# Performance work log

Measured on AMD Instinct MI355X. Metric: run time of the kernel, lower is better.

Reference implementation:

```python
import jax, jax.numpy as jnp
import numpy as np

B, C, M = 64, 64, 8192
EPS = 1e-05

def setup_inputs() -> dict:
    key = jax.random.key(0)
    x = jax.random.normal(key, (B, C, M), dtype=jnp.float32)
    return {"x": x}

def _mT(a):
    return jnp.swapaxes(a, -1, -2)

def reference(x):
    b, c, m = x.shape
    mu = x.mean(axis=2, keepdims=True)
    xc = x - mu
    cov = (xc @ _mT(xc)) / m                      # (B,C,C)
    # RBLW shrinkage
    I = jnp.eye(c, dtype=x.dtype)[None]
    trace = jnp.trace(cov, axis1=-2, axis2=-1)[:, None, None]
    second_trace = jnp.einsum('bij,bji->b', cov, cov)[:, None, None]
    numerator = (m - 2) / m * second_trace + trace ** 2
    denominator = (m + 2) * (second_trace - trace ** 2 / c)
    rho = jnp.minimum(numerator / denominator, 1.0)
    F_hat = trace / c * I
    cov = rho * F_hat + (1 - rho) * cov + EPS * I
    # eigen decomposition (no-grad in original)
    covs = jax.lax.stop_gradient(cov)
    U, L, _ = jnp.linalg.svd(covs)                # U:(B,C,C) L:(B,C) descending
    ratio = jnp.cumsum(L, axis=1) / jnp.sum(L, axis=1, keepdims=True)
    conds = jnp.any(ratio >= 1 - EPS, axis=0) | jnp.any(L <= EPS, axis=0)  # (C,)
    counter = jnp.where(jnp.any(conds), jnp.argmax(conds), c)
    # iterative rank-1 eigen refinement + deflation via scan with break mask
    Ucols = jnp.moveaxis(U, 2, 0)[..., None]      # (C,B,C,1)
    Lcols = L.T                                    # (C,B)
    S0 = jnp.zeros_like(cov)

    def step(carry, inp):
        cov_c, S_hat, active = carry
        v, Lj, j = inp                            # v:(B,C,1), Lj:(B,)
        step_active = active & (j < counter)
        # power_layer forward is identity on v
        vt = _mT(v)
        lam = (vt @ cov_c @ v) / (vt @ v)         # (B,1,1)
        Lj = Lj[:, None, None]
        ok = step_active & (~jnp.any(lam < 0)) & (~jnp.any(jnp.abs(lam - Lj) / Lj > 0.1))
        lam_safe = jnp.where(ok, lam, jnp.ones_like(lam))
        vvT = v @ vt
        S_hat = S_hat + jnp.where(ok, jax.lax.rsqrt(lam_safe) * vvT, 0.0)
        cov_c = jnp.where(ok, cov_c - cov_c @ vvT, cov_c)
        return (cov_c, S_hat, ok), None

    (_, S_hat, _), _ = jax.lax.scan(step, (cov, S0, jnp.array(True)),
                                    (Ucols, Lcols, jnp.arange(c)))
    Z = S_hat @ xc
    return Z
```

## Files before the change

kernel.cpp:

```cpp
#include <hip/hip_runtime.h>
#include <math.h>

#define BB 64
#define CCH 64
#define MMH 8192
#define SLICES 8
#define KSL 1024
#define KCH 128
#define TMZ 64
constexpr double EPSV = 1e-5;

typedef __attribute__((ext_vector_type(8))) short bf16x8;
typedef __attribute__((ext_vector_type(8))) unsigned short u16x8;
typedef __attribute__((ext_vector_type(16))) float floatx16;

__global__ __launch_bounds__(256, 2) void k1_partG(const float* __restrict__ x,
                                                   float* __restrict__ Gpart,
                                                   float* __restrict__ rspart) {
  __shared__ unsigned short h1[64][KCH + 8], h2[64][KCH + 8], h3[64][KCH + 8];
  __shared__ float rred[64][4];
  const int tid = threadIdx.x;
  const int b = blockIdx.x / SLICES;
  const int s = blockIdx.x % SLICES;
  const int row = tid >> 2;
  const int seg = (tid & 3) * 32;
  const int wv = tid >> 6;
  const int lane = tid & 63;
  const int rw = wv >> 1, cw = wv & 1;
  const int mrow = 32 * rw + (lane & 31);
  const int ncol = 32 * cw + (lane & 31);
  const int koff = (lane >> 5) * 8;
  const float* xb = x + (size_t)b * CCH * MMH + (size_t)s * KSL;
  floatx16 acc = {};
  float rsum = 0.f;
  for (int c = 0; c < KSL / KCH; ++c) {
    const float* xp = xb + (size_t)row * MMH + c * KCH + seg;
    float v[32];
#pragma unroll
    for (int q = 0; q < 8; ++q) {
      float4 t = *(const float4*)(xp + 4 * q);
      v[4 * q] = t.x;
      v[4 * q + 1] = t.y;
      v[4 * q + 2] = t.z;
      v[4 * q + 3] = t.w;
    }
#pragma unroll
    for (int o = 0; o < 32; ++o) rsum += v[o];
#pragma unroll
    for (int g = 0; g < 4; ++g) {
      u16x8 a1, a2, a3;
#pragma unroll
      for (int j = 0; j < 8; ++j) {
        float f = v[8 * g + j];
        unsigned u = __float_as_uint(f);
        unsigned short q1 = (unsigned short)(u >> 16);
        float r1 = f - __uint_as_float(u & 0xffff0000u);
        unsigned u1 = __float_as_uint(r1);
        unsigned short q2 = (unsigned short)(u1 >> 16);
        float r2 = r1 - __uint_as_float(u1 & 0xffff0000u);
        unsigned short q3 = (unsigned short)(__float_as_uint(r2) >> 16);
        a1[j] = q1;
        a2[j] = q2;
        a3[j] = q3;
      }
      *(u16x8*)&h1[row][seg + 8 * g] = a1;
      *(u16x8*)&h2[row][seg + 8 * g] = a2;
      *(u16x8*)&h3[row][seg + 8 * g] = a3;
    }
    __syncthreads();
#pragma unroll
    for (int ks = 0; ks < KCH / 16; ++ks) {
      const int kk = ks * 16 + koff;
      bf16x8 A1 = *(const bf16x8*)&h1[mrow][kk];
      bf16x8 A2 = *(const bf16x8*)&h2[mrow][kk];
      bf16x8 A3 = *(const bf16x8*)&h3[mrow][kk];
      bf16x8 B1 = *(const bf16x8*)&h1[ncol][kk];
      bf16x8 B2 = *(const bf16x8*)&h2[ncol][kk];
      bf16x8 B3 = *(const bf16x8*)&h3[ncol][kk];
      acc = __builtin_amdgcn_mfma_f32_32x32x16_bf16(A1, B1, acc, 0, 0, 0);
      acc = __builtin_amdgcn_mfma_f32_32x32x16_bf16(A1, B2, acc, 0, 0, 0);
      acc = __builtin_amdgcn_mfma_f32_32x32x16_bf16(A2, B1, acc, 0, 0, 0);
      acc = __builtin_amdgcn_mfma_f32_32x32x16_bf16(A2, B2, acc, 0, 0, 0);
      acc = __builtin_amdgcn_mfma_f32_32x32x16_bf16(A1, B3, acc, 0, 0, 0);
      acc = __builtin_amdgcn_mfma_f32_32x32x16_bf16(A3, B1, acc, 0, 0, 0);
    }
    __syncthreads();
  }
  float* gp = Gpart + ((size_t)(b * SLICES + s)) * 4096;
#pragma unroll
  for (int r = 0; r < 16; ++r) {
    int row32 = (r & 3) + 8 * (r >> 2) + 4 * (lane >> 5);
    gp[(32 * rw + row32) * 64 + 32 * cw + (lane & 31)] = acc[r];
  }
  rred[row][tid & 3] = rsum;
  __syncthreads();
  if (tid < 64) {
    rspart[((size_t)(b * SLICES + s)) * 64 + tid] =
        rred[tid][0] + rred[tid][1] + rred[tid][2] + rred[tid][3];
  }
}

__global__ __launch_bounds__(256) void k2_reduce(const float* __restrict__ Gpart,
                                                 const float* __restrict__ rspart,
                                                 float* __restrict__ cov32,
                                                 float* __restrict__ mu32,
                                                 double* __restrict__ scal) {
  __shared__ double muS[64];
  __shared__ double red[256];
  const int tid = threadIdx.x;
  const int b = blockIdx.x;
  if (tid < 64) {
    double r = 0.0;
    for (int s = 0; s < SLICES; ++s) r += (double)rspart[((size_t)(b * SLICES + s)) * 64 + tid];
    double mu = r / (double)MMH;
    muS[tid] = mu;
    mu32[b * 64 + tid] = (float)mu;
  }
  __syncthreads();
  const int base = tid * 16;
  const int i = tid >> 2;
  double g[16];
#pragma unroll
  for (int e = 0; e < 16; ++e) g[e] = 0.0;
  for (int s = 0; s < SLICES; ++s) {
    const float* gp = Gpart + ((size_t)(b * SLICES + s)) * 4096 + base;
#pragma unroll
    for (int q = 0; q < 4; ++q) {
      float4 t = *(const float4*)(gp + 4 * q);
      g[4 * q] += (double)t.x;
      g[4 * q + 1] += (double)t.y;
      g[4 * q + 2] += (double)t.z;
      g[4 * q + 3] += (double)t.w;
    }
  }
  double t1 = 0.0, t2 = 0.0;
#pragma unroll
  for (int e = 0; e < 16; ++e) {
    int j = (base + e) & 63;
    double cv = g[e] / (double)MMH - muS[i] * muS[j];
    cov32[(size_t)b * 4096 + base + e] = (float)cv;
    if (i == j) t1 += cv;
    t2 += cv * cv;
  }
  red[tid] = t1;
  __syncthreads();
  for (int st = 128; st > 0; st >>= 1) {
    if (tid < st) red[tid] += red[tid + st];
    __syncthreads();
  }
  double T1 = red[0];
  __syncthreads();
  red[tid] = t2;
  __syncthreads();
  for (int st = 128; st > 0; st >>= 1) {
    if (tid < st) red[tid] += red[tid + st];
    __syncthreads();
  }
  double T2 = red[0];
  if (tid == 0) {
    double num = ((double)(MMH - 2) / (double)MMH) * T2 + T1 * T1;
    double den = (double)(MMH + 2) * (T2 - T1 * T1 / (double)CCH);
    double r = num / den;
    double rho = (r < 1.0) ? r : 1.0;
    scal[b * 4 + 0] = rho;
    scal[b * 4 + 1] = T1 / (double)CCH;
    scal[b * 4 + 2] = 1.0 - rho;
    scal[b * 4 + 3] = (r >= 1.0) ? 1.0 : 0.0;
  }
}

__device__ __forceinline__ void gemm_acc(const float (*A)[64], const float (*B)[64],
                                         int i0, int j0, float acc[4][4]) {
#pragma unroll
  for (int a = 0; a < 4; ++a)
#pragma unroll
    for (int c = 0; c < 4; ++c) acc[a][c] = 0.f;
#pragma unroll 4
  for (int k = 0; k < 64; ++k) {
    const float4 av = *(const float4*)&A[k][i0];
    const float4 bv = *(const float4*)&B[k][j0];
    const float aa[4] = {av.x, av.y, av.z, av.w};
    const float bb[4] = {bv.x, bv.y, bv.z, bv.w};
#pragma unroll
    for (int a = 0; a < 4; ++a)
#pragma unroll
      for (int c = 0; c < 4; ++c) acc[a][c] = fmaf(aa[a], bb[c], acc[a][c]);
  }
}

__global__ __launch_bounds__(256) void k3_eig(const float* __restrict__ cov32,
                                              const double* __restrict__ scal,
                                              const float* __restrict__ mu32,
                                              float* __restrict__ SxG,
                                              float* __restrict__ smuA,
                                              float* __restrict__ vS,
                                              float* __restrict__ wvm) {
  __shared__ float As[64][64];
  __shared__ float Xs[64][64];
  __shared__ float Bs[64][64];
  __shared__ float red[64];
  __shared__ float vSh[64];
  __shared__ float ySh[64];
  __shared__ float muS[64];
  const int tid = threadIdx.x;
  const int b = blockIdx.x & 63;
  const int role = blockIdx.x >> 6;
  const double rho = scal[b * 4 + 0];
  const double alpha0 = scal[b * 4 + 1];
  const int clipped = (scal[b * 4 + 3] != 0.0);
  const float invsqc = (float)(1.0 / sqrt(alpha0 + EPSV));
  const int i0 = (tid >> 4) << 2, j0 = (tid & 15) << 2;
  float acc[4][4];
  if (tid < 64) muS[tid] = mu32[b * 64 + tid];

  if (role == 0) {
    if (clipped) {
      for (int k = tid; k < 4096; k += 256) {
        int i = k >> 6, j = k & 63;
        SxG[(size_t)b * 4096 + k] = (i == j) ? invsqc : 0.f;
      }
      if (tid < 64) smuA[b * 64 + tid] = invsqc * muS[tid];
      return;
    }
    const float orhoc = (float)((1.0 - rho) / (alpha0 + EPSV));
    const float dtermc = (float)((rho * alpha0 + EPSV) / (alpha0 + EPSV));
    for (int k = tid; k < 4096; k += 256) {
      int i = k >> 6, j = k & 63;
      float a = cov32[(size_t)b * 4096 + k];
      As[i][j] = a;
      float t = orhoc * a + ((i == j) ? dtermc : 0.f);
      Xs[i][j] = ((i == j) ? 1.5f : 0.f) - 0.5f * t;
    }
    __syncthreads();
    for (int it = 0; it < 4; ++it) {
      gemm_acc(Xs, Xs, i0, j0, acc);
#pragma unroll
      for (int a = 0; a < 4; ++a)
#pragma unroll
        for (int c = 0; c < 4; ++c) Bs[i0 + a][j0 + c] = acc[a][c];
      __syncthreads();
      gemm_acc(As, Bs, i0, j0, acc);
      float bold[4][4];
#pragma unroll
      for (int a = 0; a < 4; ++a)
#pragma unroll
        for (int c = 0; c < 4; ++c) bold[a][c] = Bs[i0 + a][j0 + c];
      __syncthreads();
#pragma unroll
      for (int a = 0; a < 4; ++a)
#pragma unroll
        for (int c = 0; c < 4; ++c) Bs[i0 + a][j0 + c] = orhoc * acc[a][c] + dtermc * bold[a][c];
      __syncthreads();
      gemm_acc(Xs, Bs, i0, j0, acc);
      float xold[4][4];
#pragma unroll
      for (int a = 0; a < 4; ++a)
#pragma unroll
        for (int c = 0; c < 4; ++c) xold[a][c] = Xs[i0 + a][j0 + c];
      __syncthreads();
#pragma unroll
      for (int a = 0; a < 4; ++a)
#pragma unroll
        for (int c = 0; c < 4; ++c) Xs[i0 + a][j0 + c] = 1.5f * xold[a][c] - 0.5f * acc[a][c];
      __syncthreads();
    }
    for (int k = tid; k < 4096; k += 256) SxG[(size_t)b * 4096 + k] = Xs[k >> 6][k & 63] * invsqc;
    if (tid < 64) {
      float sm = 0.f;
      for (int j = 0; j < 64; ++j) sm += Xs[j][tid] * muS[j];
      smuA[b * 64 + tid] = sm * invsqc;
    }
  } else {
    if (clipped) {
      if (tid < 64) vS[b * 64 + tid] = (tid == 63) ? 1.f : 0.f;
      if (tid == 0) {
        wvm[b * 2] = invsqc;
        wvm[b * 2 + 1] = mu32[b * 64 + 63];
      }
      return;
    }
    for (int k = tid; k < 4096; k += 256) As[k >> 6][k & 63] = cov32[(size_t)b * 4096 + k];
    __syncthreads();
    if (tid < 64) {
      float s = 0.f;
      for (int j = 0; j < 64; ++j) {
        float v = As[j][tid];
        s += (j == tid) ? v : fabsf(v);
      }
      red[tid] = s;
    }
    __syncthreads();
    float sig = 0.f;
    for (int j = 0; j < 64; ++j) sig = fmaxf(sig, red[j]);
    __syncthreads();
#pragma unroll
    for (int a = 0; a < 4; ++a)
#pragma unroll
      for (int c = 0; c < 4; ++c) {
        int i = i0 + a, j = j0 + c;
        Bs[i][j] = ((i == j) ? sig : 0.f) - As[i][j];
      }
    if (i0 == j0)
      red[tid >> 4] = Bs[i0][j0] + Bs[i0 + 1][j0 + 1] + Bs[i0 + 2][j0 + 2] + Bs[i0 + 3][j0 + 3];
    __syncthreads();
    for (int s5 = 0; s5 < 18; ++s5) {
      float t = 0.f;
      for (int j = 0; j < 16; ++j) t += red[j];
      float scale = 1.f / (t * t);
      gemm_acc(Bs, Bs, i0, j0, acc);
      __syncthreads();
#pragma unroll
      for (int a = 0; a < 4; ++a)
#pragma unroll
        for (int c = 0; c < 4; ++c) Bs[i0 + a][j0 + c] = acc[a][c] * scale;
      if (i0 == j0)
        red[tid >> 4] = (acc[0][0] + acc[1][1] + acc[2][2] + acc[3][3]) * scale;
      __syncthreads();
    }
    int jstar = 0;
    float best = -1.f;
    for (int j = 0; j < 64; ++j) {
      float d = Bs[j][j];
      if (d > best) {
        best = d;
        jstar = j;
      }
    }
    if (tid < 64) vSh[tid] = Bs[jstar][tid];
    __syncthreads();
    if (tid < 64) {
      float s = 0.f;
      for (int j = 0; j < 64; ++j) s += As[j][tid] * vSh[j];
      ySh[tid] = s;
    }
    __syncthreads();
    float vy = 0.f, vv = 0.f;
    for (int j = 0; j < 64; ++j) {
      vy += vSh[j] * ySh[j];
      vv += vSh[j] * vSh[j];
    }
    float lam = vy / vv;
    float lampr = (float)(rho * alpha0 + EPSV) + (float)(1.0 - rho) * lam;
    float w = 1.f / sqrtf(lampr);
    float invn = 1.f / sqrtf(vv);
    if (tid < 64) vS[b * 64 + tid] = vSh[tid] * invn;
    if (tid == 0) {
      float vmu = 0.f;
      for (int j = 0; j < 64; ++j) vmu += vSh[j] * invn * muS[j];
      wvm[b * 2] = w;
      wvm[b * 2 + 1] = vmu;
    }
  }
}

__global__ __launch_bounds__(256, 4) void k7_z(const float* __restrict__ x,
                                               const float* __restrict__ SxG,
                                               const float* __restrict__ smuA,
                                               const float* __restrict__ vS,
                                               const float* __restrict__ wvm,
                                               float* __restrict__ z) {
  __shared__ float Ss[64][68];
  __shared__ float xsv[64][64];
  __shared__ float vsh[64];
  __shared__ float smsh[64];
  const int tid = threadIdx.x;
  const int b = blockIdx.y;
  const int t0 = blockIdx.x * TMZ;
  {
    const float* sp = SxG + (size_t)b * 4096 + tid * 16;
    int i = tid >> 2, js = (tid & 3) * 16;
#pragma unroll
    for (int q = 0; q < 4; ++q) *(float4*)&Ss[i][js + 4 * q] = *(const float4*)(sp + 4 * q);
  }
  if (tid < 64) vsh[tid] = vS[b * 64 + tid];
  const float* xb = x + (size_t)b * CCH * MMH + t0;
  {
#pragma unroll
    for (int q = 0; q < 4; ++q) {
      int id = q * 256 + tid;
      int r = id >> 4, c4 = id & 15;
      float4 v = *(const float4*)(xb + (size_t)r * MMH + 4 * c4);
      int p0 = ((2 * c4 + r) & 31) * 2;
      int p1 = ((2 * c4 + 1 + r) & 31) * 2;
      *(float2*)&xsv[r][p0] = make_float2(v.x, v.y);
      *(float2*)&xsv[r][p1] = make_float2(v.z, v.w);
    }
  }
  __syncthreads();
  const float w = wvm[b * 2], vmu = wvm[b * 2 + 1];
  {
    int i = tid >> 2, js = (tid & 3) * 16;
    float wvi = w * vsh[i];
#pragma unroll
    for (int e = 0; e < 16; ++e) Ss[i][js + e] -= wvi * vsh[js + e];
  }
  if (tid < 64) smsh[tid] = smuA[b * 64 + tid] - w * vsh[tid] * vmu;
  __syncthreads();
  const int tr = tid >> 5, tc = tid & 31;
  const int i0 = tr * 8;
  float acc[8][2];
#pragma unroll
  for (int i = 0; i < 8; ++i) {
    acc[i][0] = 0.f;
    acc[i][1] = 0.f;
  }
#pragma unroll 4
  for (int k = 0; k < 64; ++k) {
    float4 s0 = *(const float4*)&Ss[k][i0];
    float4 s1 = *(const float4*)&Ss[k][i0 + 4];
    float2 xv = *(const float2*)&xsv[k][((tc + k) & 31) * 2];
    const float sa[8] = {s0.x, s0.y, s0.z, s0.w, s1.x, s1.y, s1.z, s1.w};
#pragma unroll
    for (int i = 0; i < 8; ++i) {
      acc[i][0] = fmaf(sa[i], xv.x, acc[i][0]);
      acc[i][1] = fmaf(sa[i], xv.y, acc[i][1]);
    }
  }
#pragma unroll
  for (int i = 0; i < 8; ++i) {
    float sm = smsh[i0 + i];
    float2 o = make_float2(acc[i][0] - sm, acc[i][1] - sm);
    *(float2*)(z + ((size_t)b * CCH + i0 + i) * MMH + t0 + tc * 2) = o;
  }
}

extern "C" void kernel_launch(void* const* d_in, const int* in_sizes, int n_in,
                              void* d_out, int out_size, void* d_ws, size_t ws_size,
                              hipStream_t stream) {
  (void)in_sizes;
  (void)n_in;
  (void)out_size;
  (void)ws_size;
  const float* x = (const float*)d_in[0];
  float* z = (float*)d_out;
  float* Gpart = (float*)d_out;
  float* rspart = (float*)((char*)d_out + 8388608);
  char* ws = (char*)d_ws;
  float* cov32 = (float*)(ws + 0);
  float* mu32 = (float*)(ws + 1048576);
  double* scal = (double*)(ws + 1064960);
  float* SxG = (float*)(ws + 1067008);
  float* smuA = (float*)(ws + 2115584);
  float* vS = (float*)(ws + 2131968);
  float* wvm = (float*)(ws + 2148352);

  k1_partG<<<dim3(BB * SLICES), dim3(256), 0, stream>>>(x, Gpart, rspart);
  k2_reduce<<<dim3(BB), dim3(256), 0, stream>>>(Gpart, rspart, cov32, mu32, scal);
  k3_eig<<<dim3(2 * BB), dim3(256), 0, stream>>>(cov32, scal, mu32, SxG, smuA, vS, wvm);
  k7_z<<<dim3(MMH / TMZ, BB), dim3(256), 0, stream>>>(x, SxG, smuA, vS, wvm, z);
}
```

Baseline: 338.7 us.

## Move Z projection onto bf16x3 split MFMA and raise k1 occupancy

```diff
diff --git a/kernel.cpp b/kernel.cpp
--- a/kernel.cpp
+++ b/kernel.cpp
@@ -7,14 +7,25 @@
 #define SLICES 8
 #define KSL 1024
 #define KCH 128
-#define TMZ 64
+#define TNB 128
 constexpr double EPSV = 1e-5;
 
 typedef __attribute__((ext_vector_type(8))) short bf16x8;
 typedef __attribute__((ext_vector_type(8))) unsigned short u16x8;
 typedef __attribute__((ext_vector_type(16))) float floatx16;
 
-__global__ __launch_bounds__(256, 2) void k1_partG(const float* __restrict__ x,
+__device__ __forceinline__ void split3(float f, unsigned short& q1, unsigned short& q2,
+                                       unsigned short& q3) {
+  unsigned u = __float_as_uint(f);
+  q1 = (unsigned short)(u >> 16);
+  float r1 = f - __uint_as_float(u & 0xffff0000u);
+  unsigned u1 = __float_as_uint(r1);
+  q2 = (unsigned short)(u1 >> 16);
+  float r2 = r1 - __uint_as_float(u1 & 0xffff0000u);
+  q3 = (unsigned short)(__float_as_uint(r2) >> 16);
+}
+
+__global__ __launch_bounds__(256, 3) void k1_partG(const float* __restrict__ x,
                                                    float* __restrict__ Gpart,
                                                    float* __restrict__ rspart) {
   __shared__ unsigned short h1[64][KCH + 8], h2[64][KCH + 8], h3[64][KCH + 8];
@@ -51,14 +62,8 @@
       u16x8 a1, a2, a3;
 #pragma unroll
       for (int j = 0; j < 8; ++j) {
-        float f = v[8 * g + j];
-        unsigned u = __float_as_uint(f);
-        unsigned short q1 = (unsigned short)(u >> 16);
-        float r1 = f - __uint_as_float(u & 0xffff0000u);
-        unsigned u1 = __float_as_uint(r1);
-        unsigned short q2 = (unsigned short)(u1 >> 16);
-        float r2 = r1 - __uint_as_float(u1 & 0xffff0000u);
-        unsigned short q3 = (unsigned short)(__float_as_uint(r2) >> 16);
+        unsigned short q1, q2, q3;
+        split3(v[8 * g + j], q1, q2, q3);
         a1[j] = q1;
         a2[j] = q2;
         a3[j] = q3;
@@ -359,68 +364,76 @@
                                                const float* __restrict__ vS,
                                                const float* __restrict__ wvm,
                                                float* __restrict__ z) {
-  __shared__ float Ss[64][68];
-  __shared__ float xsv[64][64];
+  __shared__ unsigned short S1[64][80], S2[64][80], S3[64][80];
   __shared__ float vsh[64];
   __shared__ float smsh[64];
   const int tid = threadIdx.x;
   const int b = blockIdx.y;
-  const int t0 = blockIdx.x * TMZ;
+  const int t0 = blockIdx.x * TNB;
+  const float w = wvm[b * 2], vmu = wvm[b * 2 + 1];
+  if (tid < 64) vsh[tid] = vS[b * 64 + tid];
+  __syncthreads();
   {
-    const float* sp = SxG + (size_t)b * 4096 + tid * 16;
-    int i = tid >> 2, js = (tid & 3) * 16;
-#pragma unroll
-    for (int q = 0; q < 4; ++q) *(float4*)&Ss[i][js + 4 * q] = *(const float4*)(sp + 4 * q);
-  }
-  if (tid < 64) vsh[tid] = vS[b * 64 + tid];
-  const float* xb = x + (size_t)b * CCH * MMH + t0;
-  {
-#pragma unroll
-    for (int q = 0; q < 4; ++q) {
-      int id = q * 256 + tid;
-      int r = id >> 4, c4 = id & 15;
-      float4 v = *(const float4*)(xb + (size_t)r * MMH + 4 * c4);
-      int p0 = ((2 * c4 + r) & 31) * 2;
-      int p1 = ((2 * c4 + 1 + r) & 31) * 2;
-      *(float2*)&xsv[r][p0] = make_float2(v.x, v.y);
-      *(float2*)&xsv[r][p1] = make_float2(v.z, v.w);
-    }
-  }
-  __syncthreads();
-  const float w = wvm[b * 2], vmu = wvm[b * 2 + 1];
-  {
-    int i = tid >> 2, js = (tid & 3) * 16;
-    float wvi = w * vsh[i];
-#pragma unroll
-    for (int e = 0; e < 16; ++e) Ss[i][js + e] -= wvi * vsh[js + e];
+    const int i = tid >> 2, js = (tid & 3) * 16;
+    const float wvi = w * vsh[i];
+    const float* sp = SxG + (size_t)b * 4096 + i * 64 + js;
+#pragma unroll
+    for (int e = 0; e < 16; ++e) {
+      float sv = sp[e] - wvi * vsh[js + e];
+      unsigned short q1, q2, q3;
+      split3(sv, q1, q2, q3);
+      S1[i][js + e] = q1;
+      S2[i][js + e] = q2;
+      S3[i][js + e] = q3;
+    }
   }
   if (tid < 64) smsh[tid] = smuA[b * 64 + tid] - w * vsh[tid] * vmu;
   __syncthreads();
-  const int tr = tid >> 5, tc = tid & 31;
-  const int i0 = tr * 8;
-  float acc[8][2];
-#pragma unroll
-  for (int i = 0; i < 8; ++i) {
-    acc[i][0] = 0.f;
-    acc[i][1] = 0.f;
-  }
-#pragma unroll 4
-  for (int k = 0; k < 64; ++k) {
-    float4 s0 = *(const float4*)&Ss[k][i0];
-    float4 s1 = *(const float4*)&Ss[k][i0 + 4];
-    float2 xv = *(const float2*)&xsv[k][((tc + k) & 31) * 2];
-    const float sa[8] = {s0.x, s0.y, s0.z, s0.w, s1.x, s1.y, s1.z, s1.w};
-#pragma unroll
-    for (int i = 0; i < 8; ++i) {
-      acc[i][0] = fmaf(sa[i], xv.x, acc[i][0]);
-      acc[i][1] = fmaf(sa[i], xv.y, acc[i][1]);
-    }
-  }
-#pragma unroll
-  for (int i = 0; i < 8; ++i) {
-    float sm = smsh[i0 + i];
-    float2 o = make_float2(acc[i][0] - sm, acc[i][1] - sm);
-    *(float2*)(z + ((size_t)b * CCH + i0 + i) * MMH + t0 + tc * 2) = o;
+  const int wv = tid >> 6, lane = tid & 63;
+  const int arow = lane & 31;
+  const int krow = (lane >> 5) * 8;
+  const int col0 = t0 + wv * 32 + (lane & 31);
+  const float* xb = x + (size_t)b * CCH * MMH;
+  floatx16 acc0 = {}, acc1 = {};
+#pragma unroll
+  for (int ks = 0; ks < 4; ++ks) {
+    const int kb = ks * 16 + krow;
+    float r0[8];
+#pragma unroll
+    for (int j = 0; j < 8; ++j) r0[j] = xb[(size_t)(kb + j) * MMH + col0];
+    bf16x8 B1, B2, B3;
+#pragma unroll
+    for (int j = 0; j < 8; ++j) {
+      unsigned short q1, q2, q3;
+      split3(r0[j], q1, q2, q3);
+      B1[j] = (short)q1;
+      B2[j] = (short)q2;
+      B3[j] = (short)q3;
+    }
+    bf16x8 A1a = *(const bf16x8*)&S1[arow][kb];
+    bf16x8 A2a = *(const bf16x8*)&S2[arow][kb];
+    bf16x8 A3a = *(const bf16x8*)&S3[arow][kb];
+    bf16x8 A1b = *(const bf16x8*)&S1[arow + 32][kb];
+    bf16x8 A2b = *(const bf16x8*)&S2[arow + 32][kb];
+    bf16x8 A3b = *(const bf16x8*)&S3[arow + 32][kb];
+    acc0 = __builtin_amdgcn_mfma_f32_32x32x16_bf16(A1a, B1, acc0, 0, 0, 0);
+    acc0 = __builtin_amdgcn_mfma_f32_32x32x16_bf16(A1a, B2, acc0, 0, 0, 0);
+    acc0 = __builtin_amdgcn_mfma_f32_32x32x16_bf16(A2a, B1, acc0, 0, 0, 0);
+    acc0 = __builtin_amdgcn_mfma_f32_32x32x16_bf16(A2a, B2, acc0, 0, 0, 0);
+    acc0 = __builtin_amdgcn_mfma_f32_32x32x16_bf16(A1a, B3, acc0, 0, 0, 0);
+    acc0 = __builtin_amdgcn_mfma_f32_32x32x16_bf16(A3a, B1, acc0, 0, 0, 0);
+    acc1 = __builtin_amdgcn_mfma_f32_32x32x16_bf16(A1b, B1, acc1, 0, 0, 0);
+    acc1 = __builtin_amdgcn_mfma_f32_32x32x16_bf16(A1b, B2, acc1, 0, 0, 0);
+    acc1 = __builtin_amdgcn_mfma_f32_32x32x16_bf16(A2b, B1, acc1, 0, 0, 0);
+    acc1 = __builtin_amdgcn_mfma_f32_32x32x16_bf16(A2b, B2, acc1, 0, 0, 0);
+    acc1 = __builtin_amdgcn_mfma_f32_32x32x16_bf16(A1b, B3, acc1, 0, 0, 0);
+    acc1 = __builtin_amdgcn_mfma_f32_32x32x16_bf16(A3b, B1, acc1, 0, 0, 0);
+  }
+#pragma unroll
+  for (int r = 0; r < 16; ++r) {
+    const int grow = (r & 3) + 8 * (r >> 2) + 4 * (lane >> 5);
+    z[((size_t)b * CCH + grow) * MMH + col0] = acc0[r] - smsh[grow];
+    z[((size_t)b * CCH + grow + 32) * MMH + col0] = acc1[r] - smsh[grow + 32];
   }
 }
 
@@ -447,5 +460,5 @@
   k1_partG<<<dim3(BB * SLICES), dim3(256), 0, stream>>>(x, Gpart, rspart);
   k2_reduce<<<dim3(BB), dim3(256), 0, stream>>>(Gpart, rspart, cov32, mu32, scal);
   k3_eig<<<dim3(2 * BB), dim3(256), 0, stream>>>(cov32, scal, mu32, SxG, smuA, vS, wvm);
-  k7_z<<<dim3(MMH / TMZ, BB), dim3(256), 0, stream>>>(x, SxG, smuA, vS, wvm, z);
-}
+  k7_z<<<dim3(MMH / TNB, BB), dim3(256), 0, stream>>>(x, SxG, smuA, vS, wvm, z);
+}
```

Measured after the change: 317.1 us. -6.4%, faster.
